# Optimization experiments

Measured on AMD Instinct MI355X. Metric: run time of the kernel, lower is better.

The kernel has to match this reference:

```python
import jax, jax.numpy as jnp
import numpy as np

B, S, H, NH = 4, 1024, 2048, 32
HD = H // NH
EPS = 1e-5

def layer_norm(x, w, b):
    mu = jnp.mean(x, axis=-1, keepdims=True)
    var = jnp.mean(jnp.square(x - mu), axis=-1, keepdims=True)
    return (x - mu) * jax.lax.rsqrt(var + EPS) * w + b

def setup_inputs() -> dict:
    key = jax.random.key(0)
    ks = jax.random.split(key, 8)
    s = 0.02
    inp = {
        'hidden_states': jax.random.normal(ks[0], (B, S, H), jnp.float32),
        'mask': jnp.tril(jnp.ones((S, S), jnp.float32))[None, None],  # causal 0/1
        'ln1_w': jnp.ones((H,), jnp.float32), 'ln1_b': jnp.zeros((H,), jnp.float32),
        'w_qkv': s * jax.random.normal(ks[1], (H, 3 * H), jnp.float32),
        'b_qkv': jnp.zeros((3 * H,), jnp.float32),
        'w_dense': s * jax.random.normal(ks[2], (H, H), jnp.float32),
        'b_dense': jnp.zeros((H,), jnp.float32),
        'ln3_w': jnp.ones((H,), jnp.float32), 'ln3_b': jnp.zeros((H,), jnp.float32),
        'ln2_w': jnp.ones((H,), jnp.float32), 'ln2_b': jnp.zeros((H,), jnp.float32),
        'w_h4h': s * jax.random.normal(ks[3], (H, 4 * H), jnp.float32),
        'b_h4h': jnp.zeros((4 * H,), jnp.float32),
        'w_4hh': s * jax.random.normal(ks[4], (4 * H, H), jnp.float32),
        'b_4hh': jnp.zeros((H,), jnp.float32),
        'ln4_w': jnp.ones((H,), jnp.float32), 'ln4_b': jnp.zeros((H,), jnp.float32),
    }
    return inp

def _layer(hidden_states, mask, ln1_w, ln1_b, w_qkv, b_qkv, w_dense, b_dense,
           ln3_w, ln3_b, ln2_w, ln2_b, w_h4h, b_h4h, w_4hh, b_4hh, ln4_w, ln4_b):
    # --- input LN ---
    x1 = layer_norm(hidden_states, ln1_w, ln1_b)
    # --- self attention ---
    qkv = x1 @ w_qkv + b_qkv                              # [B,S,3H]
    q, k, v = jnp.split(qkv, 3, axis=-1)
    def heads(t):  # [B,S,H] -> [B,NH,S,HD]
        return t.reshape(B, S, NH, HD).transpose(0, 2, 1, 3)
    q, k, v = heads(q), heads(k), heads(v)
    scores = jnp.einsum('bnqd,bnkd->bnqk', q / jnp.sqrt(jnp.float32(HD)), k)
    scores = scores * mask - 10000.0 * (1.0 - mask)
    probs = jax.nn.softmax(scores, axis=-1)
    ctx = jnp.einsum('bnqk,bnkd->bnqd', probs, v)
    ctx = ctx.transpose(0, 2, 1, 3).reshape(B, S, H)
    attn_out = ctx @ w_dense + b_dense
    # sandwich LN on attention output
    attn_out = layer_norm(attn_out, ln3_w, ln3_b)
    ln_input = hidden_states + attn_out
    # --- MLP ---
    x2 = layer_norm(ln_input, ln2_w, ln2_b)
    inter = jax.nn.gelu(x2 @ w_h4h + b_h4h, approximate=True)
    mlp_out = inter @ w_4hh + b_4hh
    mlp_out = layer_norm(mlp_out, ln4_w, ln4_b)
    return ln_input + mlp_out

def reference(hidden_states, mask, ln1_w, ln1_b, w_qkv, b_qkv, w_dense, b_dense,
              ln3_w, ln3_b, ln2_w, ln2_b, w_h4h, b_h4h, w_4hh, b_4hh, ln4_w, ln4_b):
    return _layer(hidden_states, mask, ln1_w, ln1_b, w_qkv, b_qkv, w_dense, b_dense,
                  ln3_w, ln3_b, ln2_w, ln2_b, w_h4h, b_h4h, w_4hh, b_4hh, ln4_w, ln4_b)
```

## Files before the change

### kernel.cpp

```cpp
#include <hip/hip_runtime.h>
#include <cstdint>
#include <cstddef>

typedef __bf16 bf16_t;
typedef __bf16 bf16x8 __attribute__((ext_vector_type(8)));
typedef float f32x4 __attribute__((ext_vector_type(4)));

#define BB 4
#define SS 1024
#define HH 2048
#define NHH 32
#define HDD 64
#define MTOK 4096
#define QKVLD 6144

static constexpr size_t OFF_WQKV   = 0;
static constexpr size_t OFF_WDENSE = 25165824;
static constexpr size_t OFF_WH4H   = 33554432;
static constexpr size_t OFF_W4HH   = 67108864;
static constexpr size_t OFF_X1     = 100663296;
static constexpr size_t OFF_QKV    = 117440512;
static constexpr size_t OFF_ATTND2 = 150994944;
static constexpr size_t OFF_VT     = 167772160;
static constexpr size_t OFF_LNIN   = 184549376;
static constexpr size_t OFF_MLP    = 218103808;
static constexpr size_t OFF_MLP2   = 0;

__device__ __forceinline__ uint16_t f2bfu(float f) {
  union { float f; uint32_t u; } v; v.f = f;
  return (uint16_t)((v.u + 0x7FFFu + ((v.u >> 16) & 1u)) >> 16);
}
__device__ __forceinline__ bf16_t f2bf(float f) {
  union { uint16_t u; bf16_t b; } o; o.u = f2bfu(f);
  return o.b;
}

__device__ __forceinline__ void g2l16(const void* g, void* l) {
  __builtin_amdgcn_global_load_lds(
      (const __attribute__((address_space(1))) void*)g,
      (__attribute__((address_space(3))) void*)l, 16, 0, 0);
}

__global__ void convert_transpose_kernel(const float* __restrict__ W, bf16_t* __restrict__ WT,
                                         int K, int N) {
  __shared__ float t[32][33];
  const int n0 = blockIdx.x * 32;
  const int k0 = blockIdx.y * 32;
  const int tx = threadIdx.x, ty = threadIdx.y;
#pragma unroll
  for (int j = 0; j < 4; ++j)
    t[ty + j * 8][tx] = W[(size_t)(k0 + ty + j * 8) * N + n0 + tx];
  __syncthreads();
#pragma unroll
  for (int j = 0; j < 4; ++j)
    WT[(size_t)(n0 + ty + j * 8) * K + k0 + tx] = f2bf(t[tx][ty + j * 8]);
}

__global__ void transpose_v_kernel(const bf16_t* __restrict__ qkv, bf16_t* __restrict__ vT) {
  __shared__ bf16_t t[32][33];
  const int s0 = blockIdx.x * 32;
  const int d0 = blockIdx.y * 32;
  const int bh = blockIdx.z;
  const int b = bh >> 5, h = bh & 31;
  const int tx = threadIdx.x, ty = threadIdx.y;
  const bf16_t* src = qkv + (size_t)b * SS * QKVLD + 2 * HH + h * HDD;
#pragma unroll
  for (int j = 0; j < 4; ++j)
    t[ty + j * 8][tx] = src[(size_t)(s0 + ty + j * 8) * QKVLD + d0 + tx];
  __syncthreads();
  bf16_t* dst = vT + (size_t)bh * HDD * SS;
#pragma unroll
  for (int j = 0; j < 4; ++j)
    dst[(size_t)(d0 + ty + j * 8) * SS + s0 + tx] = t[tx][ty + j * 8];
}

__device__ __forceinline__ void block_reduce2(float& s, float& ss) {
#pragma unroll
  for (int o = 32; o > 0; o >>= 1) {
    s += __shfl_down(s, o, 64);
    ss += __shfl_down(ss, o, 64);
  }
  __shared__ float red[8];
  const int wave = threadIdx.x >> 6;
  const int lane = threadIdx.x & 63;
  if (lane == 0) { red[wave] = s; red[4 + wave] = ss; }
  __syncthreads();
  s = red[0] + red[1] + red[2] + red[3];
  ss = red[4] + red[5] + red[6] + red[7];
  __syncthreads();
}

__device__ __forceinline__ void load8(const float* base, int tid, float* v) {
  float4 a = ((const float4*)base)[tid];
  float4 b = ((const float4*)base)[tid + 256];
  v[0] = a.x; v[1] = a.y; v[2] = a.z; v[3] = a.w;
  v[4] = b.x; v[5] = b.y; v[6] = b.z; v[7] = b.w;
}
__device__ __forceinline__ void store8f(float* base, int tid, const float* v) {
  ((float4*)base)[tid] = make_float4(v[0], v[1], v[2], v[3]);
  ((float4*)base)[tid + 256] = make_float4(v[4], v[5], v[6], v[7]);
}
__device__ __forceinline__ void store8bf(bf16_t* base, int tid, const float* v) {
  ushort4 o0 = {f2bfu(v[0]), f2bfu(v[1]), f2bfu(v[2]), f2bfu(v[3])};
  ushort4 o1 = {f2bfu(v[4]), f2bfu(v[5]), f2bfu(v[6]), f2bfu(v[7])};
  ((ushort4*)base)[tid] = o0;
  ((ushort4*)base)[tid + 256] = o1;
}
__device__ __forceinline__ void row_stats(const float* v, float& mean, float& inv) {
  float s = 0.f, ss = 0.f;
#pragma unroll
  for (int i = 0; i < 8; ++i) { s += v[i]; ss += v[i] * v[i]; }
  block_reduce2(s, ss);
  mean = s * (1.0f / 2048.0f);
  float var = ss * (1.0f / 2048.0f) - mean * mean;
  inv = rsqrtf(var + 1e-5f);
}

__global__ __launch_bounds__(256) void ln1_kernel(const float* __restrict__ x,
                                                  const float* __restrict__ w,
                                                  const float* __restrict__ b,
                                                  bf16_t* __restrict__ out) {
  const int row = blockIdx.x, tid = threadIdx.x;
  float v[8], wv[8], bv[8], o[8];
  load8(x + (size_t)row * HH, tid, v);
  float mean, inv;
  row_stats(v, mean, inv);
  load8(w, tid, wv);
  load8(b, tid, bv);
#pragma unroll
  for (int i = 0; i < 8; ++i) o[i] = (v[i] - mean) * inv * wv[i] + bv[i];
  store8bf(out + (size_t)row * HH, tid, o);
}

__global__ __launch_bounds__(256) void fuse_mid_kernel(
    const float* __restrict__ ad, const float* __restrict__ ad2,
    const float* __restrict__ hid,
    const float* __restrict__ w3, const float* __restrict__ b3,
    const float* __restrict__ w2, const float* __restrict__ b2,
    float* __restrict__ lnin, bf16_t* __restrict__ x2) {
  const int row = blockIdx.x, tid = threadIdx.x;
  float a[8], a2[8], h[8], wv[8], bv[8], l[8], o[8];
  load8(ad + (size_t)row * HH, tid, a);
  load8(ad2 + (size_t)row * HH, tid, a2);
#pragma unroll
  for (int i = 0; i < 8; ++i) a[i] += a2[i];
  float mean3, inv3;
  row_stats(a, mean3, inv3);
  load8(hid + (size_t)row * HH, tid, h);
  load8(w3, tid, wv);
  load8(b3, tid, bv);
#pragma unroll
  for (int i = 0; i < 8; ++i) l[i] = h[i] + (a[i] - mean3) * inv3 * wv[i] + bv[i];
  store8f(lnin + (size_t)row * HH, tid, l);
  float mean2, inv2;
  row_stats(l, mean2, inv2);
  load8(w2, tid, wv);
  load8(b2, tid, bv);
#pragma unroll
  for (int i = 0; i < 8; ++i) o[i] = (l[i] - mean2) * inv2 * wv[i] + bv[i];
  store8bf(x2 + (size_t)row * HH, tid, o);
}

__global__ __launch_bounds__(256) void fuse_out_kernel(
    const float* __restrict__ mlp, const float* __restrict__ mlp2,
    const float* __restrict__ lnin,
    const float* __restrict__ w4, const float* __restrict__ b4,
    float* __restrict__ out) {
  const int row = blockIdx.x, tid = threadIdx.x;
  float m[8], m2[8], l[8], wv[8], bv[8], o[8];
  load8(mlp + (size_t)row * HH, tid, m);
  load8(mlp2 + (size_t)row * HH, tid, m2);
#pragma unroll
  for (int i = 0; i < 8; ++i) m[i] += m2[i];
  float mean4, inv4;
  row_stats(m, mean4, inv4);
  load8(lnin + (size_t)row * HH, tid, l);
  load8(w4, tid, wv);
  load8(b4, tid, bv);
#pragma unroll
  for (int i = 0; i < 8; ++i) o[i] = l[i] + (m[i] - mean4) * inv4 * wv[i] + bv[i];
  store8f(out + (size_t)row * HH, tid, o);
}

#define MFMA16(a, b, cc) __builtin_amdgcn_mfma_f32_16x16x32_bf16(a, b, cc, 0, 0, 0)

#define STAGE(ISB, BUF, HALF, KT) do {                                              \
    const char* _s = ((ISB) ? bS : aS) + (size_t)(HALF) * h128 + (size_t)(KT) * 128; \
    char* _d = lds + ((ISB) ? 65536 : 0) + (BUF) * 32768 + (HALF) * 16384 +         \
               wave * 1024;                                                         \
    g2l16(_s, _d);                                                                  \
    g2l16(_s + h64, _d + 8192);                                                     \
  } while (0)

#define LDA(BUF, MQ)                                                                \
  _Pragma("unroll") for (int mf = 0; mf < 4; ++mf) {                                \
    const char* _p = aRd + (BUF) * 32768 + (MQ) * 8192 + mf * 2048;                 \
    aR[mf * 2]     = *(const bf16x8*)(_p + colK0);                                  \
    aR[mf * 2 + 1] = *(const bf16x8*)(_p + colK1);                                  \
  }

#define LDB(BR, BUF, NQ)                                                            \
  _Pragma("unroll") for (int nf = 0; nf < 2; ++nf) {                                \
    const char* _p = bRd + (BUF) * 32768 + (NQ) * 4096 + nf * 2048;                 \
    BR[nf * 2]     = *(const bf16x8*)(_p + colK0);                                  \
    BR[nf * 2 + 1] = *(const bf16x8*)(_p + colK1);                                  \
  }

#define MMA(MQ, NQ, BR)                                                             \
  _Pragma("unroll") for (int mf = 0; mf < 4; ++mf)                                  \
  _Pragma("unroll") for (int nf = 0; nf < 2; ++nf)                                  \
  _Pragma("unroll") for (int ks = 0; ks < 2; ++ks)                                  \
    acc[(MQ) * 4 + mf][(NQ) * 2 + nf] =                                             \
        MFMA16(aR[mf * 2 + ks], BR[nf * 2 + ks], acc[(MQ) * 4 + mf][(NQ) * 2 + nf]);

#define BARS()                                                                      \
  __builtin_amdgcn_s_barrier();                                                     \
  __builtin_amdgcn_s_setprio(1);

#define ENDP()                                                                      \
  __builtin_amdgcn_s_setprio(0);                                                    \
  __builtin_amdgcn_s_barrier();

template <int EPI, int SPLITK>
__global__ __launch_bounds__(512, 2) void gemm256(
    const bf16_t* __restrict__ A, const bf16_t* __restrict__ BT,
    const float* __restrict__ bias, void* __restrict__ out0, void* __restrict__ out1,
    const int M, const int N, const int Keff, const int ldK) {
  __shared__ alignas(16) char lds[131072];
  const int tid = threadIdx.x;
  const int wave = tid >> 6, lane = tid & 63;
  const int wm = wave >> 2, wn = wave & 3;
  const int c = lane & 15, g = lane >> 4;

  const int nwg = gridDim.x;
  int bid = (blockIdx.x & 7) * (nwg >> 3) + (blockIdx.x >> 3);
  const int nm = M >> 8;
  int slice = 0;
  if (SPLITK == 2) {
    const int per = nm * (N >> 8);
    slice = bid >= per;
    bid -= slice * per;
  }
  const int mt = bid % nm, nt = bid / nm;

  const size_t ldb = (size_t)ldK * 2;
  const size_t h64 = (size_t)64 * ldb;
  const size_t h128 = 2 * h64;
  const char* aPan = (const char*)A + (size_t)(mt * 256) * ldb + (size_t)(slice * Keff) * 2;
  const char* bPan = (const char*)BT + (size_t)(nt * 256) * ldb + (size_t)(slice * Keff) * 2;

  const int srow = tid >> 3;
  const int scb = ((tid & 7) << 4) ^ ((srow & 7) << 4);
  const char* aS = aPan + (size_t)srow * ldb + scb;
  const char* bS = bPan + (size_t)srow * ldb + scb;

  const int x4 = (c & 7) << 4;
  const int colK0 = (g * 16) ^ x4;
  const int colK1 = (64 + g * 16) ^ x4;
  const char* aRd = lds + wm * 16384 + c * 128;
  const char* bRd = lds + 65536 + (wn >> 1) * 16384 + ((wn & 1) * 64 + c) * 128;

  f32x4 acc[8][4] = {};
  bf16x8 aR[8], b0R[4], b1R[4];

  const int NITER = Keff >> 7;
  const int NT2 = NITER * 2;

  STAGE(1, 0, 0, 0); STAGE(1, 0, 1, 0); STAGE(0, 0, 0, 0); STAGE(0, 0, 1, 0);
  STAGE(1, 1, 0, 1); STAGE(1, 1, 1, 1);
  asm volatile("s_waitcnt vmcnt(4)" ::: "memory");
  __builtin_amdgcn_s_barrier();

  for (int it = 0; it < NITER; ++it) {
    const int ktb = 2 * it + 1;
    int kt2 = 2 * it + 2; if (kt2 >= NT2) kt2 = 0;
    int kt3 = 2 * it + 3; if (kt3 >= NT2) kt3 = 0;
    LDA(0, 0); LDB(b0R, 0, 0); STAGE(0, 1, 0, ktb);
    BARS(); MMA(0, 0, b0R); ENDP();
    LDB(b1R, 0, 1); STAGE(0, 1, 1, ktb);
    BARS(); MMA(0, 1, b1R); ENDP();
    LDA(0, 1); STAGE(1, 0, 0, kt2);
    BARS(); MMA(1, 1, b1R); ENDP();
    STAGE(1, 0, 1, kt2);
    asm volatile("s_waitcnt vmcnt(4)" ::: "memory");
    BARS(); MMA(1, 0, b0R); ENDP();
    LDA(1, 0); LDB(b0R, 1, 0); STAGE(0, 0, 0, kt2);
    BARS(); MMA(0, 0, b0R); ENDP();
    LDB(b1R, 1, 1); STAGE(0, 0, 1, kt2);
    BARS(); MMA(0, 1, b1R); ENDP();
    LDA(1, 1); STAGE(1, 1, 0, kt3);
    BARS(); MMA(1, 1, b1R); ENDP();
    STAGE(1, 1, 1, kt3);
    asm volatile("s_waitcnt vmcnt(4)" ::: "memory");
    BARS(); MMA(1, 0, b0R); ENDP();
  }

  const int rowb = mt * 256 + wm * 128 + g * 4;
  const int colb = nt * 256 + wn * 64 + c;
  if constexpr (EPI == 0) {
    float* o = (float*)(slice ? out1 : out0);
#pragma unroll
    for (int nf = 0; nf < 4; ++nf) {
      const int col = colb + nf * 16;
      const float bv = (slice == 0) ? bias[col] : 0.0f;
#pragma unroll
      for (int mf = 0; mf < 8; ++mf) {
        const int r = rowb + mf * 16;
#pragma unroll
        for (int e = 0; e < 4; ++e)
          o[(size_t)(r + e) * N + col] = acc[mf][nf][e] + bv;
      }
    }
  } else if constexpr (EPI == 1) {
    bf16_t* o = (bf16_t*)out0;
#pragma unroll
    for (int nf = 0; nf < 4; ++nf) {
      const int col = colb + nf * 16;
      const float bv = bias[col];
#pragma unroll
      for (int mf = 0; mf < 8; ++mf) {
        const int r = rowb + mf * 16;
#pragma unroll
        for (int e = 0; e < 4; ++e)
          o[(size_t)(r + e) * N + col] = f2bf(acc[mf][nf][e] + bv);
      }
    }
  } else {
    bf16_t* o = (bf16_t*)out0;
#pragma unroll
    for (int nf = 0; nf < 4; ++nf) {
      const int col = colb + nf * 16;
      const float bv = bias[col];
#pragma unroll
      for (int mf = 0; mf < 8; ++mf) {
        const int r = rowb + mf * 16;
#pragma unroll
        for (int e = 0; e < 4; ++e) {
          float u = acc[mf][nf][e] + bv;
          float cc2 = 0.7978845608f * (u + 0.044715f * u * u * u);
          float ex = __expf(2.0f * cc2);
          float th = 1.0f - 2.0f / (ex + 1.0f);
          o[(size_t)(r + e) * N + col] = f2bf(0.5f * u * (1.0f + th));
        }
      }
    }
  }
}

__global__ __launch_bounds__(512) void attn_kernel(
    const bf16_t* __restrict__ qkv, const bf16_t* __restrict__ vT,
    bf16_t* __restrict__ ctx) {
  __shared__ alignas(16) char Ksm[8192];
  __shared__ alignas(16) char Vsm[8192];
  __shared__ alignas(16) char Psm[16384];

  const int id = blockIdx.x;
  const int qt = 7 - (id >> 7);
  const int bh = id & 127;
  const int b = bh >> 5, h = bh & 31;
  const int tid = threadIdx.x;
  const int wave = tid >> 6;
  const int lane = tid & 63;
  const int q0 = qt * 128;
  const int q0w = q0 + wave * 16;
  const int c = lane & 15;
  const int g = lane >> 4;

  const bf16_t* qb = qkv + ((size_t)b * SS + q0w) * QKVLD + h * HDD;
  const bf16x8 qa0 = *(const bf16x8*)(qb + (size_t)c * QKVLD + g * 8);
  const bf16x8 qa1 = *(const bf16x8*)(qb + (size_t)c * QKVLD + 32 + g * 8);

  f32x4 o[4] = {};
  float mrow[4], lrow[4];
#pragma unroll
  for (int e = 0; e < 4; ++e) { mrow[e] = -1e30f; lrow[e] = 0.0f; }

  const int sr = tid >> 3;
  const int sgb = ((tid & 7) * 16) ^ ((sr & 7) << 4);
  const char* kgb = (const char*)(qkv + (size_t)b * SS * QKVLD + HH + h * HDD);
  const char* vgb = (const char*)(vT + (size_t)bh * HDD * SS);
  char* kdst = Ksm + wave * 1024;
  char* vdst = Vsm + wave * 1024;
  char* Pw = Psm + wave * 2048;

  const int ntiles = (q0 + 128) >> 6;

  for (int t = 0; t < ntiles; ++t) {
    const int kb = t * 64;
    g2l16(kgb + (size_t)(kb + sr) * (QKVLD * 2) + sgb, kdst);
    g2l16(vgb + (size_t)sr * 2048 + (size_t)kb * 2 + sgb, vdst);
    __syncthreads();

    if (kb < q0w + 16) {
      f32x4 s[4] = {};
#pragma unroll
      for (int sub = 0; sub < 4; ++sub) {
        const int n = sub * 16 + c;
        const int x = (n & 7) << 4;
        bf16x8 kf0 = *(const bf16x8*)(Ksm + n * 128 + ((g * 16) ^ x));
        bf16x8 kf1 = *(const bf16x8*)(Ksm + n * 128 + ((64 + g * 16) ^ x));
        s[sub] = MFMA16(qa0, kf0, s[sub]);
        s[sub] = MFMA16(qa1, kf1, s[sub]);
      }
      const bool diag = (kb + 63 > q0w);
      float pv[4][4];
#pragma unroll
      for (int sub = 0; sub < 4; ++sub)
#pragma unroll
        for (int e = 0; e < 4; ++e) {
          float sv = s[sub][e] * 0.125f;
          if (diag && (kb + sub * 16 + c > q0w + g * 4 + e)) sv = -10000.0f;
          pv[sub][e] = sv;
        }
      float scale[4];
#pragma unroll
      for (int e = 0; e < 4; ++e) {
        float mx = fmaxf(fmaxf(pv[0][e], pv[1][e]), fmaxf(pv[2][e], pv[3][e]));
        mx = fmaxf(mx, __shfl_xor(mx, 1, 64));
        mx = fmaxf(mx, __shfl_xor(mx, 2, 64));
        mx = fmaxf(mx, __shfl_xor(mx, 4, 64));
        mx = fmaxf(mx, __shfl_xor(mx, 8, 64));
        const float mnew = fmaxf(mrow[e], mx);
        scale[e] = __expf(mrow[e] - mnew);
        mrow[e] = mnew;
      }
#pragma unroll
      for (int e = 0; e < 4; ++e) {
        const int row = g * 4 + e;
        const int xr = (row & 7) << 4;
        float sum = 0.0f;
#pragma unroll
        for (int sub = 0; sub < 4; ++sub) {
          float p = __expf(pv[sub][e] - mrow[e]);
          sum += p;
          const int cb = (sub * 16 + c) * 2;
          *(bf16_t*)(Pw + row * 128 + (cb ^ xr)) = f2bf(p);
        }
        sum += __shfl_xor(sum, 1, 64);
        sum += __shfl_xor(sum, 2, 64);
        sum += __shfl_xor(sum, 4, 64);
        sum += __shfl_xor(sum, 8, 64);
        lrow[e] = lrow[e] * scale[e] + sum;
      }
#pragma unroll
      for (int d = 0; d < 4; ++d)
#pragma unroll
        for (int e = 0; e < 4; ++e) o[d][e] *= scale[e];
      const int xa = (c & 7) << 4;
      bf16x8 pa0 = *(const bf16x8*)(Pw + c * 128 + ((g * 16) ^ xa));
      bf16x8 pa1 = *(const bf16x8*)(Pw + c * 128 + ((64 + g * 16) ^ xa));
#pragma unroll
      for (int d = 0; d < 4; ++d) {
        const int n = d * 16 + c;
        const int xv = (n & 7) << 4;
        bf16x8 vf0 = *(const bf16x8*)(Vsm + n * 128 + ((g * 16) ^ xv));
        bf16x8 vf1 = *(const bf16x8*)(Vsm + n * 128 + ((64 + g * 16) ^ xv));
        o[d] = MFMA16(pa0, vf0, o[d]);
        o[d] = MFMA16(pa1, vf1, o[d]);
      }
    }
    __syncthreads();
  }

#pragma unroll
  for (int e = 0; e < 4; ++e) {
    const int qrow = q0w + g * 4 + e;
    const float inv = 1.0f / lrow[e];
#pragma unroll
    for (int d = 0; d < 4; ++d)
      ctx[((size_t)b * SS + qrow) * HH + h * 64 + d * 16 + c] = f2bf(o[d][e] * inv);
  }
}

extern "C" void kernel_launch(void* const* d_in, const int* in_sizes, int n_in,
                              void* d_out, int out_size, void* d_ws, size_t ws_size,
                              hipStream_t stream) {
  const float* hidden = (const float*)d_in[0];
  const float* ln1w = (const float*)d_in[2];
  const float* ln1b = (const float*)d_in[3];
  const float* wqkv = (const float*)d_in[4];
  const float* bqkv = (const float*)d_in[5];
  const float* wdense = (const float*)d_in[6];
  const float* bdense = (const float*)d_in[7];
  const float* ln3w = (const float*)d_in[8];
  const float* ln3b = (const float*)d_in[9];
  const float* ln2w = (const float*)d_in[10];
  const float* ln2b = (const float*)d_in[11];
  const float* wh4h = (const float*)d_in[12];
  const float* bh4h = (const float*)d_in[13];
  const float* w4hh = (const float*)d_in[14];
  const float* b4hh = (const float*)d_in[15];
  const float* ln4w = (const float*)d_in[16];
  const float* ln4b = (const float*)d_in[17];

  char* ws = (char*)d_ws;
  bf16_t* wqkvT = (bf16_t*)(ws + OFF_WQKV);
  bf16_t* wdenseT = (bf16_t*)(ws + OFF_WDENSE);
  bf16_t* wh4hT = (bf16_t*)(ws + OFF_WH4H);
  bf16_t* w4hhT = (bf16_t*)(ws + OFF_W4HH);
  bf16_t* x1 = (bf16_t*)(ws + OFF_X1);
  bf16_t* qkv = (bf16_t*)(ws + OFF_QKV);
  bf16_t* vT = (bf16_t*)(ws + OFF_VT);
  bf16_t* ctx = (bf16_t*)(ws + OFF_X1);
  float* attnd = (float*)(ws + OFF_QKV);
  float* attnd2 = (float*)(ws + OFF_ATTND2);
  float* lnin = (float*)(ws + OFF_LNIN);
  bf16_t* x2 = (bf16_t*)(ws + OFF_X1);
  bf16_t* inter = (bf16_t*)(ws + OFF_QKV);
  float* mlp = (float*)(ws + OFF_MLP);
  float* mlp2 = (float*)(ws + OFF_MLP2);

  dim3 tb(32, 8);
  convert_transpose_kernel<<<dim3(6144 / 32, 2048 / 32), tb, 0, stream>>>(wqkv, wqkvT, 2048, 6144);
  convert_transpose_kernel<<<dim3(2048 / 32, 2048 / 32), tb, 0, stream>>>(wdense, wdenseT, 2048, 2048);
  convert_transpose_kernel<<<dim3(8192 / 32, 2048 / 32), tb, 0, stream>>>(wh4h, wh4hT, 2048, 8192);
  convert_transpose_kernel<<<dim3(2048 / 32, 8192 / 32), tb, 0, stream>>>(w4hh, w4hhT, 8192, 2048);

  ln1_kernel<<<MTOK, 256, 0, stream>>>(hidden, ln1w, ln1b, x1);

  gemm256<1, 1><<<dim3((6144 / 256) * (4096 / 256)), 512, 0, stream>>>(
      x1, wqkvT, bqkv, (void*)qkv, nullptr, MTOK, 6144, 2048, 2048);

  transpose_v_kernel<<<dim3(SS / 32, HDD / 32, BB * NHH), tb, 0, stream>>>(qkv, vT);

  attn_kernel<<<dim3(1024), 512, 0, stream>>>(qkv, vT, ctx);

  gemm256<0, 2><<<dim3((2048 / 256) * (4096 / 256) * 2), 512, 0, stream>>>(
      ctx, wdenseT, bdense, (void*)attnd, (void*)attnd2, MTOK, 2048, 1024, 2048);

  fuse_mid_kernel<<<MTOK, 256, 0, stream>>>(attnd, attnd2, hidden, ln3w, ln3b, ln2w, ln2b, lnin, x2);

  gemm256<2, 1><<<dim3((8192 / 256) * (4096 / 256)), 512, 0, stream>>>(
      x2, wh4hT, bh4h, (void*)inter, nullptr, MTOK, 8192, 2048, 2048);

  gemm256<0, 2><<<dim3((2048 / 256) * (4096 / 256) * 2), 512, 0, stream>>>(
      inter, w4hhT, b4hh, (void*)mlp, (void*)mlp2, MTOK, 2048, 4096, 8192);

  fuse_out_kernel<<<MTOK, 256, 0, stream>>>(mlp, mlp2, lnin, ln4w, ln4b, (float*)d_out);
}
```

Measured before the change: 638.5 us.

## Merge GEMM main-loop phases from eight to four per iteration

Restructures the 256x256 GEMM main loop so each iteration runs four barrier-delimited phases instead of eight. Each phase loads both B fragments and issues two stage copies before a larger MFMA cluster, and the MFMA loop order now puts the k-step outermost. The goal is less barrier and setprio overhead and longer uninterrupted MFMA runs. In exchange, the global-to-LDS copies land in bigger bursts and interleave less finely with compute, and both b0R and b1R stay live at the same time, which raises register pressure.

After: 647.6 us. Within noise of the previous version (+1.4%).

```diff
diff --git a/kernel.cpp b/kernel.cpp
--- a/kernel.cpp
+++ b/kernel.cpp
@@ -207,9 +207,9 @@
   }
 
 #define MMA(MQ, NQ, BR)                                                             \
+  _Pragma("unroll") for (int ks = 0; ks < 2; ++ks)                                  \
   _Pragma("unroll") for (int mf = 0; mf < 4; ++mf)                                  \
   _Pragma("unroll") for (int nf = 0; nf < 2; ++nf)                                  \
-  _Pragma("unroll") for (int ks = 0; ks < 2; ++ks)                                  \
     acc[(MQ) * 4 + mf][(NQ) * 2 + nf] =                                             \
         MFMA16(aR[mf * 2 + ks], BR[nf * 2 + ks], acc[(MQ) * 4 + mf][(NQ) * 2 + nf]);
 
@@ -220,6 +220,8 @@
 #define ENDP()                                                                      \
   __builtin_amdgcn_s_setprio(0);                                                    \
   __builtin_amdgcn_s_barrier();
+
+#define VM4() asm volatile("s_waitcnt vmcnt(4)" ::: "memory")
 
 template <int EPI, int SPLITK>
 __global__ __launch_bounds__(512, 2) void gemm256(
@@ -266,33 +268,30 @@
   const int NITER = Keff >> 7;
   const int NT2 = NITER * 2;
 
-  STAGE(1, 0, 0, 0); STAGE(1, 0, 1, 0); STAGE(0, 0, 0, 0); STAGE(0, 0, 1, 0);
+  STAGE(1, 0, 0, 0); STAGE(1, 0, 1, 0);
+  STAGE(0, 0, 0, 0); STAGE(0, 0, 1, 0);
   STAGE(1, 1, 0, 1); STAGE(1, 1, 1, 1);
-  asm volatile("s_waitcnt vmcnt(4)" ::: "memory");
+  VM4();
   __builtin_amdgcn_s_barrier();
 
   for (int it = 0; it < NITER; ++it) {
-    const int ktb = 2 * it + 1;
-    int kt2 = 2 * it + 2; if (kt2 >= NT2) kt2 = 0;
-    int kt3 = 2 * it + 3; if (kt3 >= NT2) kt3 = 0;
-    LDA(0, 0); LDB(b0R, 0, 0); STAGE(0, 1, 0, ktb);
-    BARS(); MMA(0, 0, b0R); ENDP();
-    LDB(b1R, 0, 1); STAGE(0, 1, 1, ktb);
-    BARS(); MMA(0, 1, b1R); ENDP();
-    LDA(0, 1); STAGE(1, 0, 0, kt2);
-    BARS(); MMA(1, 1, b1R); ENDP();
-    STAGE(1, 0, 1, kt2);
-    asm volatile("s_waitcnt vmcnt(4)" ::: "memory");
-    BARS(); MMA(1, 0, b0R); ENDP();
-    LDA(1, 0); LDB(b0R, 1, 0); STAGE(0, 0, 0, kt2);
-    BARS(); MMA(0, 0, b0R); ENDP();
-    LDB(b1R, 1, 1); STAGE(0, 0, 1, kt2);
-    BARS(); MMA(0, 1, b1R); ENDP();
-    LDA(1, 1); STAGE(1, 1, 0, kt3);
-    BARS(); MMA(1, 1, b1R); ENDP();
-    STAGE(1, 1, 1, kt3);
-    asm volatile("s_waitcnt vmcnt(4)" ::: "memory");
-    BARS(); MMA(1, 0, b0R); ENDP();
+    const int kt1 = 2 * it + 1;
+    int kt0n = 2 * it + 2; if (kt0n >= NT2) kt0n -= NT2;
+    int kt1n = 2 * it + 3; if (kt1n >= NT2) kt1n -= NT2;
+    LDA(0, 0); LDB(b0R, 0, 0); LDB(b1R, 0, 1);
+    STAGE(0, 1, 0, kt1); STAGE(0, 1, 1, kt1);
+    BARS(); MMA(0, 0, b0R); MMA(0, 1, b1R); ENDP();
+    LDA(0, 1);
+    STAGE(1, 0, 0, kt0n); STAGE(1, 0, 1, kt0n);
+    VM4();
+    BARS(); MMA(1, 0, b0R); MMA(1, 1, b1R); ENDP();
+    LDA(1, 0); LDB(b0R, 1, 0); LDB(b1R, 1, 1);
+    STAGE(0, 0, 0, kt0n); STAGE(0, 0, 1, kt0n);
+    BARS(); MMA(0, 0, b0R); MMA(0, 1, b1R); ENDP();
+    LDA(1, 1);
+    STAGE(1, 1, 0, kt1n); STAGE(1, 1, 1, kt1n);
+    VM4();
+    BARS(); MMA(1, 0, b0R); MMA(1, 1, b1R); ENDP();
   }
 
   const int rowb = mt * 256 + wm * 128 + g * 4;
```
